# Kernel tuning notes

Hardware: AMD Instinct MI355X
Metric: run time of the kernel (lower is better)

## Reference

```python
import jax, jax.numpy as jnp
import numpy as np

EMB = 1024
HEADS = 16
QKV = 64
INNER = 2816  # 256 * ceil(2*1024*4/3 / 256)


def rms_norm(x, w, eps=1e-6):
    xf = x.astype(jnp.float32)
    n = xf * jax.lax.rsqrt(jnp.mean(xf * xf, axis=-1, keepdims=True) + eps)
    return n.astype(x.dtype) * w


def setup_inputs() -> dict:
    key = jax.random.key(0)
    ks = jax.random.split(key, 12)
    s = 0.02
    return {
        "x": jax.random.normal(ks[0], (4, 2048, EMB), dtype=jnp.float32),
        "Wq": jax.random.normal(ks[1], (HEADS * QKV, EMB), dtype=jnp.float32) * s,
        "Wk": jax.random.normal(ks[2], (HEADS * QKV, EMB), dtype=jnp.float32) * s,
        "Wv": jax.random.normal(ks[3], (HEADS * QKV, EMB), dtype=jnp.float32) * s,
        "Wc": jax.random.normal(ks[4], (EMB, HEADS * QKV), dtype=jnp.float32) * s,
        "bc": jnp.zeros((EMB,), dtype=jnp.float32),
        "g1": jnp.ones((EMB,), dtype=jnp.float32),
        "g2": jnp.ones((EMB,), dtype=jnp.float32),
        "L1": jax.random.normal(ks[5], (INNER, EMB), dtype=jnp.float32) * s,
        "L2": jax.random.normal(ks[6], (INNER, EMB), dtype=jnp.float32) * s,
        "L3": jax.random.normal(ks[7], (EMB, INNER), dtype=jnp.float32) * s,
    }


def reference(x, Wq, Wk, Wv, Wc, bc, g1, g2, L1, L2, L3):
    B, N, D = x.shape
    # QKV projections (torch Linear: y = x @ W.T), split into heads: [B,H,N,dk]
    q = (x @ Wq.T).reshape(B, N, HEADS, QKV).transpose(0, 2, 1, 3)
    k = (x @ Wk.T).reshape(B, N, HEADS, QKV).transpose(0, 2, 1, 3)
    v = (x @ Wv.T).reshape(B, N, HEADS, QKV).transpose(0, 2, 1, 3)
    # attention: explicit score matrix [B,H,N,N]
    score = jnp.einsum("bhnd,bhmd->bhnm", q, k) / jnp.sqrt(jnp.float32(QKV))
    weights = jax.nn.softmax(score, axis=-1)
    out = jnp.einsum("bhnm,bhmd->bhnd", weights, v)
    out = out.transpose(0, 2, 1, 3).reshape(B, N, HEADS * QKV)
    mha = out @ Wc.T + bc
    h = rms_norm(x + mha, g1)
    # parallel gated MLP: silu(h@L1.T) * (h@L2.T) @ L3.T
    ff = (jax.nn.silu(h @ L1.T) * (h @ L2.T)) @ L3.T
    return rms_norm(h + ff, g2)
```

## Files before the change

kernel.cpp:

```cpp
#include <hip/hip_runtime.h>
#include <hip/hip_bf16.h>


#define EMB   1024
#define HEADS 16
#define DK    64
#define INNER 2816
#define BATCH 4
#define NTOK  2048
#define MROWS (BATCH * NTOK)

#define QSCALE 0.18033688011112042f

typedef short bf16x8 __attribute__((ext_vector_type(8)));
typedef short s16x4  __attribute__((ext_vector_type(4)));
typedef float f32x4  __attribute__((ext_vector_type(4)));

typedef const void __attribute__((address_space(1)))* gas_cvp;
typedef void       __attribute__((address_space(3)))* las_vp;

__device__ __forceinline__ short to_bf16(float f) {
  union { float f; unsigned u; } x; x.f = f;
  unsigned r = x.u + 0x7FFFu + ((x.u >> 16) & 1u);
  return (short)(r >> 16);
}

__device__ __forceinline__ float from_bf16(short s) {
  union { unsigned u; float f; } x;
  x.u = ((unsigned)(unsigned short)s) << 16;
  return x.f;
}

__device__ __forceinline__ unsigned cvt_pk_bf16(float a, float b) {
  unsigned r;
  asm("v_cvt_pk_bf16_f32 %0, %1, %2" : "=v"(r) : "v"(a), "v"(b));
  return r;
}

__device__ __forceinline__ void gld16(void* lds, const void* g) {
  __builtin_amdgcn_global_load_lds((gas_cvp)g, (las_vp)lds, 16, 0, 0);
}

__global__ __launch_bounds__(256, 4)
void cvt_all(const float* __restrict__ x,  const float* __restrict__ Wq,
             const float* __restrict__ Wk, const float* __restrict__ Wv,
             const float* __restrict__ Wc, const float* __restrict__ L1,
             const float* __restrict__ L2, const float* __restrict__ L3,
             short* __restrict__ xb, short* __restrict__ wqkv,
             short* __restrict__ wcb, short* __restrict__ l12,
             short* __restrict__ l3b)
{
  const int blk = blockIdx.x, tt = threadIdx.x;
  auto conv4 = [&](const float* s, short* d, int i) {
    float4 v = ((const float4*)s)[i];
    s16x4 o;
    o[0] = to_bf16(v.x); o[1] = to_bf16(v.y);
    o[2] = to_bf16(v.z); o[3] = to_bf16(v.w);
    ((s16x4*)d)[i] = o;
  };
  if (blk < 8192)       conv4(x,  xb,                 blk * 256 + tt);
  else if (blk < 9216)  conv4(Wq, wqkv,               (blk - 8192) * 256 + tt);
  else if (blk < 10240) conv4(Wk, wqkv + 1024 * 1024, (blk - 9216) * 256 + tt);
  else if (blk < 11264) conv4(Wv, wqkv + 2 * 1024 * 1024, (blk - 10240) * 256 + tt);
  else if (blk < 12288) conv4(Wc, wcb,                (blk - 11264) * 256 + tt);
  else if (blk < 15104) conv4(L3, l3b,                (blk - 12288) * 256 + tt);
  else {
    int i = (blk - 15104) * 256 + tt;
    int row = i >> 8, c4 = i & 255;
    float4 v1 = ((const float4*)L1)[i];
    float4 v2 = ((const float4*)L2)[i];
    s16x4 o1, o2;
    o1[0]=to_bf16(v1.x); o1[1]=to_bf16(v1.y); o1[2]=to_bf16(v1.z); o1[3]=to_bf16(v1.w);
    o2[0]=to_bf16(v2.x); o2[1]=to_bf16(v2.y); o2[2]=to_bf16(v2.z); o2[3]=to_bf16(v2.w);
    ((s16x4*)l12)[(size_t)(2 * row) * 256 + c4]     = o1;
    ((s16x4*)l12)[(size_t)(2 * row + 1) * 256 + c4] = o2;
  }
}

template<int MODE>
__global__ __launch_bounds__(256, 2)
void gemm_bt(const short* __restrict__ A, const short* __restrict__ Bw,
             int M, int N, int K,
             void* __restrict__ out0, void* __restrict__ out1,
             void* __restrict__ out2,
             const float* __restrict__ aux0, const float* __restrict__ aux1,
             const short* __restrict__ auxb)
{
  __shared__ short At[128 * 64];
  __shared__ short Bt[128 * 64];
  const int t = threadIdx.x;
  const int lane = t & 63;
  const int l15 = lane & 15, lhi = lane >> 4;
  const int w  = t >> 6;
  const int wm = (w >> 1) << 6;
  const int wn = (w & 1) << 6;
  const int chunk = gridDim.x >> 3;
  const int wg = (blockIdx.x & 7) * chunk + (blockIdx.x >> 3);
  const int tilesN = N >> 7;
  const int m0 = (wg / tilesN) << 7;
  const int n0 = (wg % tilesN) << 7;

  const int r = t >> 3;
  const int p = t & 7;
  const int psrc = p ^ (r & 7);
  const short* Ag = A  + (size_t)(m0 + r) * K + psrc * 8;
  const short* Bg = Bw + (size_t)(n0 + r) * K + psrc * 8;

  f32x4 acc[4][4];
  const f32x4 fz = {0.f, 0.f, 0.f, 0.f};
#pragma unroll
  for (int i = 0; i < 4; i++)
#pragma unroll
    for (int j = 0; j < 4; j++) acc[i][j] = fz;

  int aoff[2][4], boff[2][4];
#pragma unroll
  for (int kk = 0; kk < 2; kk++)
#pragma unroll
    for (int mt = 0; mt < 4; mt++) {
      int ra = wm + mt * 16 + l15;
      aoff[kk][mt] = ra * 128 + ((kk * 64 + lhi * 16) ^ ((ra & 7) << 4));
      int rb = wn + mt * 16 + l15;
      boff[kk][mt] = rb * 128 + ((kk * 64 + lhi * 16) ^ ((rb & 7) << 4));
    }

  for (int k0 = 0; k0 < K; k0 += 64) {
#pragma unroll
    for (int i = 0; i < 4; i++) {
      gld16((char*)At + t * 16 + i * 4096, Ag + (size_t)i * 32 * K + k0);
      gld16((char*)Bt + t * 16 + i * 4096, Bg + (size_t)i * 32 * K + k0);
    }
    __syncthreads();
#pragma unroll
    for (int kk = 0; kk < 2; kk++) {
      bf16x8 a[4], b[4];
#pragma unroll
      for (int mt = 0; mt < 4; mt++)
        a[mt] = *(const bf16x8*)((const char*)At + aoff[kk][mt]);
#pragma unroll
      for (int nt = 0; nt < 4; nt++)
        b[nt] = *(const bf16x8*)((const char*)Bt + boff[kk][nt]);
#pragma unroll
      for (int mt = 0; mt < 4; mt++)
#pragma unroll
        for (int nt = 0; nt < 4; nt++)
          acc[mt][nt] = __builtin_amdgcn_mfma_f32_16x16x32_bf16(
              a[mt], b[nt], acc[mt][nt], 0, 0, 0);
    }
    __syncthreads();
  }

#pragma unroll
  for (int mt = 0; mt < 4; mt++) {
#pragma unroll
    for (int nt = 0; nt < 4; nt++) {
      const int mb = m0 + wm + mt * 16 + lhi * 4;
      const int n  = n0 + wn + nt * 16 + l15;
      if constexpr (MODE == 0) {
        const int which = n >> 10, c = n & 1023;
        if (which == 2) {
          const int hh = c >> 6, dd = c & 63;
          const int bb = mb >> 11, tok = mb & 2047;
          s16x4 pk;
#pragma unroll
          for (int j = 0; j < 4; j++) pk[j] = to_bf16(acc[mt][nt][j]);
          *(s16x4*)((short*)out2 +
                    (size_t)((bb * HEADS + hh) * DK + dd) * NTOK + tok) = pk;
        } else {
          short* dst = (which == 0) ? (short*)out0 : (short*)out1;
          const float scl = (which == 0) ? QSCALE : 1.0f;
#pragma unroll
          for (int j = 0; j < 4; j++)
            dst[(size_t)(mb + j) * 1024 + c] = to_bf16(acc[mt][nt][j] * scl);
        }
      } else if constexpr (MODE == 1) {
#pragma unroll
        for (int j = 0; j < 4; j++) {
          size_t idx = (size_t)(mb + j) * 1024 + n;
          ((float*)out0)[idx] = acc[mt][nt][j] + aux1[n] + aux0[idx];
        }
      } else if constexpr (MODE == 2) {
#pragma unroll
        for (int j = 0; j < 4; j++) {
          float v0 = acc[mt][nt][j];
          float v1 = __shfl_xor(v0, 1);
          if ((lane & 1) == 0) {
            float su = v0 / (1.f + __expf(-v0));
            ((short*)out0)[(size_t)(mb + j) * INNER + (n >> 1)] =
                to_bf16(su * v1);
          }
        }
      } else {
#pragma unroll
        for (int j = 0; j < 4; j++) {
          size_t idx = (size_t)(mb + j) * 1024 + n;
          ((float*)out0)[idx] = acc[mt][nt][j] + from_bf16(auxb[idx]);
        }
      }
    }
  }
}

__global__ __launch_bounds__(256, 3)
void attn_k(const short* __restrict__ qb, const short* __restrict__ kb,
            const short* __restrict__ vtb, short* __restrict__ ob)
{
  __shared__ short Kt[2][64 * 64];
  __shared__ short Vt[2][64 * 64];
  __shared__ short Pt[128 * 68];
  const int t = threadIdx.x;
  const int lane = t & 63;
  const int l15 = lane & 15, lhi = lane >> 4;
  const int w = t >> 6;
  const int bh = blockIdx.x;
  const int b = bh >> 4, h = bh & 15;
  const int q0 = blockIdx.y << 7;

  bf16x8 aq[2][2];
#pragma unroll
  for (int s = 0; s < 2; s++) {
    const short* qp = qb + (size_t)(b * NTOK + q0 + w * 32 + s * 16 + l15) * EMB
                         + h * DK + lhi * 8;
    aq[s][0] = *(const bf16x8*)qp;
    aq[s][1] = *(const bf16x8*)(qp + 32);
  }

  f32x4 acc[2][4];
  const f32x4 fz = {0.f, 0.f, 0.f, 0.f};
#pragma unroll
  for (int s = 0; s < 2; s++)
#pragma unroll
    for (int dt = 0; dt < 4; dt++) acc[s][dt] = fz;
  float l_run[2] = {0.f, 0.f};

  const int r = t >> 3, p = t & 7;
  const int psrc = p ^ (r & 7);
  const short* kg = kb  + (size_t)(b * NTOK + r) * EMB + h * DK + psrc * 8;
  const short* vg = vtb + (size_t)(bh * DK + r) * NTOK + psrc * 8;

  int kvoff[4][2];
#pragma unroll
  for (int x = 0; x < 4; x++)
#pragma unroll
    for (int kk = 0; kk < 2; kk++) {
      int row = x * 16 + l15;
      kvoff[x][kk] = row * 128 + ((kk * 64 + lhi * 16) ^ ((row & 7) << 4));
    }
  int pw[2][4], pr[2][2];
#pragma unroll
  for (int s = 0; s < 2; s++) {
    const int prow = w * 32 + s * 16 + l15;
#pragma unroll
    for (int kvt = 0; kvt < 4; kvt++) pw[s][kvt] = prow * 136 + kvt * 32 + lhi * 8;
#pragma unroll
    for (int kk = 0; kk < 2; kk++)   pr[s][kk]  = prow * 136 + kk * 64 + lhi * 16;
  }

  auto stage = [&](short* Kd, short* Vd, int kv0) {
    const short* ks = kg + (size_t)kv0 * EMB;
    const short* vs = vg + kv0;
    gld16(Kd + t * 8,        ks);
    gld16(Kd + t * 8 + 2048, ks + (size_t)32 * EMB);
    gld16(Vd + t * 8,        vs);
    gld16(Vd + t * 8 + 2048, vs + (size_t)32 * NTOK);
  };

  auto do_set = [&](f32x4 (&sv)[4], float& lr, const int (&pwo)[4]) {
    float ls = 0.f;
#pragma unroll
    for (int kvt = 0; kvt < 4; kvt++)
#pragma unroll
      for (int j = 0; j < 4; j++) {
        float pe = exp2f(sv[kvt][j]);
        sv[kvt][j] = pe;
        ls += pe;
      }
    lr += ls;
#pragma unroll
    for (int kvt = 0; kvt < 4; kvt++) {
      uint2 u;
      u.x = cvt_pk_bf16(sv[kvt][0], sv[kvt][1]);
      u.y = cvt_pk_bf16(sv[kvt][2], sv[kvt][3]);
      *(uint2*)((char*)Pt + pwo[kvt]) = u;
    }
  };

  auto compute = [&](const short* Kb_, const short* Vb_) {
    const char* Kb = (const char*)Kb_;
    const char* Vb = (const char*)Vb_;
    bf16x8 kf[4][2];
#pragma unroll
    for (int x = 0; x < 4; x++)
#pragma unroll
      for (int kk = 0; kk < 2; kk++)
        kf[x][kk] = *(const bf16x8*)(Kb + kvoff[x][kk]);
    f32x4 s0[4], s1[4];
    __builtin_amdgcn_s_setprio(1);
#pragma unroll
    for (int kvt = 0; kvt < 4; kvt++) {
      s0[kvt] = __builtin_amdgcn_mfma_f32_16x16x32_bf16(kf[kvt][0], aq[0][0], fz, 0, 0, 0);
      s0[kvt] = __builtin_amdgcn_mfma_f32_16x16x32_bf16(kf[kvt][1], aq[0][1], s0[kvt], 0, 0, 0);
      s1[kvt] = __builtin_amdgcn_mfma_f32_16x16x32_bf16(kf[kvt][0], aq[1][0], fz, 0, 0, 0);
      s1[kvt] = __builtin_amdgcn_mfma_f32_16x16x32_bf16(kf[kvt][1], aq[1][1], s1[kvt], 0, 0, 0);
    }
    __builtin_amdgcn_s_setprio(0);
    do_set(s0, l_run[0], pw[0]);
    do_set(s1, l_run[1], pw[1]);
    bf16x8 vf[4][2];
#pragma unroll
    for (int dt = 0; dt < 4; dt++)
#pragma unroll
      for (int kk = 0; kk < 2; kk++)
        vf[dt][kk] = *(const bf16x8*)(Vb + kvoff[dt][kk]);
    bf16x8 pb0[2], pb1[2];
#pragma unroll
    for (int kk = 0; kk < 2; kk++) {
      pb0[kk] = *(const bf16x8*)((const char*)Pt + pr[0][kk]);
      pb1[kk] = *(const bf16x8*)((const char*)Pt + pr[1][kk]);
    }
    __builtin_amdgcn_s_setprio(1);
#pragma unroll
    for (int dt = 0; dt < 4; dt++) {
#pragma unroll
      for (int kk = 0; kk < 2; kk++)
        acc[0][dt] = __builtin_amdgcn_mfma_f32_16x16x32_bf16(vf[dt][kk], pb0[kk], acc[0][dt], 0, 0, 0);
#pragma unroll
      for (int kk = 0; kk < 2; kk++)
        acc[1][dt] = __builtin_amdgcn_mfma_f32_16x16x32_bf16(vf[dt][kk], pb1[kk], acc[1][dt], 0, 0, 0);
    }
    __builtin_amdgcn_s_setprio(0);
  };

  stage(Kt[0], Vt[0], 0);
  for (int it = 0; it < 32; it += 2) {
    stage(Kt[1], Vt[1], (it + 1) * 64);
    asm volatile("s_waitcnt vmcnt(4)" ::: "memory");
    __builtin_amdgcn_s_barrier();
    compute(Kt[0], Vt[0]);
    __builtin_amdgcn_s_barrier();
    if (it + 2 < 32) {
      stage(Kt[0], Vt[0], (it + 2) * 64);
      asm volatile("s_waitcnt vmcnt(4)" ::: "memory");
    } else {
      asm volatile("s_waitcnt vmcnt(0)" ::: "memory");
    }
    __builtin_amdgcn_s_barrier();
    compute(Kt[1], Vt[1]);
    __builtin_amdgcn_s_barrier();
  }

#pragma unroll
  for (int s = 0; s < 2; s++) {
    float lt = l_run[s];
    lt += __shfl_xor(lt, 16);
    lt += __shfl_xor(lt, 32);
    const float inv = 1.f / lt;
    short* op = ob + (size_t)(b * NTOK + q0 + w * 32 + s * 16 + l15) * EMB + h * DK;
#pragma unroll
    for (int dt = 0; dt < 4; dt++) {
      s16x4 pk;
#pragma unroll
      for (int j = 0; j < 4; j++) pk[j] = to_bf16(acc[s][dt][j] * inv);
      *(s16x4*)(op + dt * 16 + lhi * 4) = pk;
    }
  }
}

template<int OM>
__global__ __launch_bounds__(256, 4)
void rmsnorm_k(const float* __restrict__ in, const float* __restrict__ gw,
               float* __restrict__ of, short* __restrict__ ob)
{
  const int row = blockIdx.x;
  const int t = threadIdx.x;
  const float4 v = ((const float4*)(in + (size_t)row * EMB))[t];
  float ss = v.x * v.x + v.y * v.y + v.z * v.z + v.w * v.w;
#pragma unroll
  for (int off = 1; off < 64; off <<= 1) ss += __shfl_xor(ss, off);
  __shared__ float red[4];
  if ((t & 63) == 0) red[t >> 6] = ss;
  __syncthreads();
  float tot = red[0] + red[1] + red[2] + red[3];
  const float rinv = rsqrtf(tot * (1.f / EMB) + 1e-6f);
  const float4 g4 = ((const float4*)gw)[t];
  float4 o;
  o.x = v.x * rinv * g4.x; o.y = v.y * rinv * g4.y;
  o.z = v.z * rinv * g4.z; o.w = v.w * rinv * g4.w;
  if (OM == 0) {
    ((float4*)(of + (size_t)row * EMB))[t] = o;
  } else {
    s16x4 pk;
    pk[0] = to_bf16(o.x); pk[1] = to_bf16(o.y);
    pk[2] = to_bf16(o.z); pk[3] = to_bf16(o.w);
    ((s16x4*)(ob + (size_t)row * EMB))[t] = pk;
  }
}

extern "C" void kernel_launch(void* const* d_in, const int* in_sizes, int n_in,
                              void* d_out, int out_size, void* d_ws, size_t ws_size,
                              hipStream_t stream)
{
  const float* x  = (const float*)d_in[0];
  const float* Wq = (const float*)d_in[1];
  const float* Wk = (const float*)d_in[2];
  const float* Wv = (const float*)d_in[3];
  const float* Wc = (const float*)d_in[4];
  const float* bc = (const float*)d_in[5];
  const float* g1 = (const float*)d_in[6];
  const float* g2 = (const float*)d_in[7];
  const float* L1 = (const float*)d_in[8];
  const float* L2 = (const float*)d_in[9];
  const float* L3 = (const float*)d_in[10];
  float* out = (float*)d_out;

  char* ws = (char*)d_ws;
  size_t o = 0;
  auto take = [&](size_t bytes) -> char* {
    char* pp = ws + o;
    o += (bytes + 255) & ~(size_t)255;
    return pp;
  };
  short* xb   = (short*)take((size_t)MROWS * EMB * 2);
  short* wqkv = (short*)take((size_t)3072 * 1024 * 2);
  short* wcb  = (short*)take((size_t)1024 * 1024 * 2);
  short* l12  = (short*)take((size_t)5632 * 1024 * 2);
  short* l3b  = (short*)take((size_t)1024 * 2816 * 2);
  short* q    = (short*)take((size_t)MROWS * EMB * 2);
  short* k    = (short*)take((size_t)MROWS * EMB * 2);
  short* v    = (short*)take((size_t)MROWS * EMB * 2);
  short* attn = (short*)take((size_t)MROWS * EMB * 2);
  float* t1   = (float*)take((size_t)MROWS * EMB * 4);
  short* hb   = (short*)take((size_t)MROWS * EMB * 2);
  short* gated = q;
  float* t2    = t1;

  cvt_all<<<17920, 256, 0, stream>>>(x, Wq, Wk, Wv, Wc, L1, L2, L3,
                                     xb, wqkv, wcb, l12, l3b);

  gemm_bt<0><<<64 * 24, 256, 0, stream>>>(xb, wqkv, MROWS, 3072, 1024,
                                          q, k, v, nullptr, nullptr, nullptr);
  attn_k<<<dim3(64, 16), 256, 0, stream>>>(q, k, v, attn);
  gemm_bt<1><<<64 * 8, 256, 0, stream>>>(attn, wcb, MROWS, 1024, 1024,
                                         t1, nullptr, nullptr, x, bc, nullptr);
  rmsnorm_k<1><<<MROWS, 256, 0, stream>>>(t1, g1, nullptr, hb);
  gemm_bt<2><<<64 * 44, 256, 0, stream>>>(hb, l12, MROWS, 5632, 1024,
                                          gated, nullptr, nullptr,
                                          nullptr, nullptr, nullptr);
  gemm_bt<3><<<64 * 8, 256, 0, stream>>>(gated, l3b, MROWS, 1024, 2816,
                                         t2, nullptr, nullptr,
                                         nullptr, nullptr, hb);
  rmsnorm_k<0><<<MROWS, 256, 0, stream>>>(t2, g2, out, nullptr);
}
```

Baseline: 415.0 us.

## Reuse K tile as P scratch, raise attention occupancy and swizzle block mapping

The attention kernel drops its separate P staging buffer. Each wave now writes and reads its softmax probabilities in the K tile it has just loaded into registers, with a barrier after the K-fragment reads so the space is free. This cuts LDS use and lets launch bounds rise from 3 to 4 blocks per CU. The double-buffer loop becomes a single-step loop: it waits for the current tile, then issues the next tile's load before computing, so the separate wait and barrier per half-step are gone. The grid is flattened to 1D and remapped so consecutive blocks of a (batch, head) are grouped across the 8-way interleave, aiming for better K/V cache reuse. The risks are an extra barrier inside every compute step and a full vmcnt(0) wait each iteration.

```diff
diff --git a/kernel.cpp b/kernel.cpp
--- a/kernel.cpp
+++ b/kernel.cpp
@@ -201,20 +201,20 @@
   }
 }
 
-__global__ __launch_bounds__(256, 3)
+__global__ __launch_bounds__(256, 4)
 void attn_k(const short* __restrict__ qb, const short* __restrict__ kb,
             const short* __restrict__ vtb, short* __restrict__ ob)
 {
   __shared__ short Kt[2][64 * 64];
   __shared__ short Vt[2][64 * 64];
-  __shared__ short Pt[128 * 68];
   const int t = threadIdx.x;
   const int lane = t & 63;
   const int l15 = lane & 15, lhi = lane >> 4;
   const int w = t >> 6;
-  const int bh = blockIdx.x;
+  const int wg = (blockIdx.x & 7) * 128 + (blockIdx.x >> 3);
+  const int bh = wg >> 4;
   const int b = bh >> 4, h = bh & 15;
-  const int q0 = blockIdx.y << 7;
+  const int q0 = (wg & 15) << 7;
 
   bf16x8 aq[2][2];
 #pragma unroll
@@ -246,15 +246,14 @@
       int row = x * 16 + l15;
       kvoff[x][kk] = row * 128 + ((kk * 64 + lhi * 16) ^ ((row & 7) << 4));
     }
-  int pw[2][4], pr[2][2];
-#pragma unroll
-  for (int s = 0; s < 2; s++) {
-    const int prow = w * 32 + s * 16 + l15;
-#pragma unroll
-    for (int kvt = 0; kvt < 4; kvt++) pw[s][kvt] = prow * 136 + kvt * 32 + lhi * 8;
-#pragma unroll
-    for (int kk = 0; kk < 2; kk++)   pr[s][kk]  = prow * 136 + kk * 64 + lhi * 16;
-  }
+  const int prow = w * 16 + l15;
+  int pw_[4], pr_[2];
+#pragma unroll
+  for (int kvt = 0; kvt < 4; kvt++)
+    pw_[kvt] = prow * 128 + ((kvt * 32 + lhi * 8) ^ ((l15 & 7) << 4));
+#pragma unroll
+  for (int kk = 0; kk < 2; kk++)
+    pr_[kk] = prow * 128 + ((kk * 64 + lhi * 16) ^ ((l15 & 7) << 4));
 
   auto stage = [&](short* Kd, short* Vd, int kv0) {
     const short* ks = kg + (size_t)kv0 * EMB;
@@ -265,7 +264,7 @@
     gld16(Vd + t * 8 + 2048, vs + (size_t)32 * NTOK);
   };
 
-  auto do_set = [&](f32x4 (&sv)[4], float& lr, const int (&pwo)[4]) {
+  auto do_set = [&](f32x4 (&sv)[4], float& lr, char* Pb, bf16x8 (&pb)[2]) {
     float ls = 0.f;
 #pragma unroll
     for (int kvt = 0; kvt < 4; kvt++)
@@ -281,19 +280,25 @@
       uint2 u;
       u.x = cvt_pk_bf16(sv[kvt][0], sv[kvt][1]);
       u.y = cvt_pk_bf16(sv[kvt][2], sv[kvt][3]);
-      *(uint2*)((char*)Pt + pwo[kvt]) = u;
-    }
+      *(uint2*)(Pb + pw_[kvt]) = u;
+    }
+#pragma unroll
+    for (int kk = 0; kk < 2; kk++)
+      pb[kk] = *(const bf16x8*)(Pb + pr_[kk]);
   };
 
-  auto compute = [&](const short* Kb_, const short* Vb_) {
-    const char* Kb = (const char*)Kb_;
-    const char* Vb = (const char*)Vb_;
+  auto compute = [&](int cur) {
+    char* Kb = (char*)&Kt[cur][0];
+    const char* Vb = (const char*)&Vt[cur][0];
     bf16x8 kf[4][2];
 #pragma unroll
     for (int x = 0; x < 4; x++)
 #pragma unroll
       for (int kk = 0; kk < 2; kk++)
         kf[x][kk] = *(const bf16x8*)(Kb + kvoff[x][kk]);
+    asm volatile("s_waitcnt lgkmcnt(0)" ::: "memory");
+    __builtin_amdgcn_sched_barrier(0);
+    __builtin_amdgcn_s_barrier();
     f32x4 s0[4], s1[4];
     __builtin_amdgcn_s_setprio(1);
 #pragma unroll
@@ -304,20 +309,15 @@
       s1[kvt] = __builtin_amdgcn_mfma_f32_16x16x32_bf16(kf[kvt][1], aq[1][1], s1[kvt], 0, 0, 0);
     }
     __builtin_amdgcn_s_setprio(0);
-    do_set(s0, l_run[0], pw[0]);
-    do_set(s1, l_run[1], pw[1]);
+    bf16x8 pb0[2], pb1[2];
+    do_set(s0, l_run[0], Kb, pb0);
+    do_set(s1, l_run[1], Kb, pb1);
     bf16x8 vf[4][2];
 #pragma unroll
     for (int dt = 0; dt < 4; dt++)
 #pragma unroll
       for (int kk = 0; kk < 2; kk++)
         vf[dt][kk] = *(const bf16x8*)(Vb + kvoff[dt][kk]);
-    bf16x8 pb0[2], pb1[2];
-#pragma unroll
-    for (int kk = 0; kk < 2; kk++) {
-      pb0[kk] = *(const bf16x8*)((const char*)Pt + pr[0][kk]);
-      pb1[kk] = *(const bf16x8*)((const char*)Pt + pr[1][kk]);
-    }
     __builtin_amdgcn_s_setprio(1);
 #pragma unroll
     for (int dt = 0; dt < 4; dt++) {
@@ -331,22 +331,14 @@
     __builtin_amdgcn_s_setprio(0);
   };
 
-  stage(Kt[0], Vt[0], 0);
-  for (int it = 0; it < 32; it += 2) {
-    stage(Kt[1], Vt[1], (it + 1) * 64);
-    asm volatile("s_waitcnt vmcnt(4)" ::: "memory");
+  stage(&Kt[0][0], &Vt[0][0], 0);
+  for (int it = 0; it < 32; ++it) {
+    const int cur = it & 1;
+    asm volatile("s_waitcnt vmcnt(0)" ::: "memory");
     __builtin_amdgcn_s_barrier();
-    compute(Kt[0], Vt[0]);
-    __builtin_amdgcn_s_barrier();
-    if (it + 2 < 32) {
-      stage(Kt[0], Vt[0], (it + 2) * 64);
-      asm volatile("s_waitcnt vmcnt(4)" ::: "memory");
-    } else {
-      asm volatile("s_waitcnt vmcnt(0)" ::: "memory");
-    }
-    __builtin_amdgcn_s_barrier();
-    compute(Kt[1], Vt[1]);
-    __builtin_amdgcn_s_barrier();
+    if (it + 1 < 32)
+      stage(&Kt[cur ^ 1][0], &Vt[cur ^ 1][0], (it + 1) * 64);
+    compute(cur);
   }
 
 #pragma unroll
@@ -439,7 +431,7 @@
 
   gemm_bt<0><<<64 * 24, 256, 0, stream>>>(xb, wqkv, MROWS, 3072, 1024,
                                           q, k, v, nullptr, nullptr, nullptr);
-  attn_k<<<dim3(64, 16), 256, 0, stream>>>(q, k, v, attn);
+  attn_k<<<1024, 256, 0, stream>>>(q, k, v, attn);
   gemm_bt<1><<<64 * 8, 256, 0, stream>>>(attn, wcb, MROWS, 1024, 1024,
                                          t1, nullptr, nullptr, x, bc, nullptr);
   rmsnorm_k<1><<<MROWS, 256, 0, stream>>>(t1, g1, nullptr, hb);
```

Result: no change. 413.5 us (-0.4%).
